# Optimization experiments

Measured on AMD Instinct MI355X. Metric: run time of the kernel, lower is better.

Reference implementation:

```python
import jax, jax.numpy as jnp
import numpy as np

D_MODEL = 256
NUM_ENTRIES = 256 * 256 * 2  # (a, b, carry_in) table
INPUT_DIM = 2 * D_MODEL + 2


def _build_tables():
    k = np.arange(NUM_ENTRIES)
    a = k // 512
    b = (k // 2) % 256
    c = k % 2
    W1 = np.zeros((INPUT_DIM, NUM_ENTRIES), dtype=np.float32)
    W1[a, k] = 1.0
    W1[D_MODEL + b, k] = 1.0
    W1[2 * D_MODEL + c, k] = 1.0
    total = a + b + c
    W2_sum = np.zeros((NUM_ENTRIES, D_MODEL), dtype=np.float32)
    W2_sum[k, total & 255] = 1.0
    W2_carry = np.zeros((NUM_ENTRIES, 2), dtype=np.float32)
    W2_carry[k, (total >= 256).astype(np.int64)] = 1.0
    return jnp.asarray(W1), jnp.asarray(W2_sum), jnp.asarray(W2_carry)


def setup_inputs() -> dict:
    key = jax.random.key(0)
    k1, k2 = jax.random.split(key)
    W1, W2_sum, W2_carry = _build_tables()
    a_emb = jax.random.uniform(k1, (4, D_MODEL), dtype=jnp.float32)
    b_emb = jax.random.uniform(k2, (4, D_MODEL), dtype=jnp.float32)
    return {"a_emb": a_emb, "b_emb": b_emb, "W1": W1, "W2_sum": W2_sum, "W2_carry": W2_carry}


def reference(a_emb, b_emb, W1, W2_sum, W2_carry):
    # 4 sequential carry-propagation steps over the bytes of a 32-bit add.
    def step(carry, ab):
        a_i, b_i = ab  # each [D_MODEL]
        x = jnp.concatenate([a_i, b_i, carry])  # [514]
        scores = x @ W1  # [131072] matvec against full table
        weights = jax.nn.softmax((scores - 2.5) * 10.0)  # sharp soft one-hot
        result = weights @ W2_sum   # [D_MODEL]
        new_carry = weights @ W2_carry  # [2]
        return new_carry, result

    carry0 = jnp.zeros(2, dtype=a_emb.dtype).at[0].set(1.0)
    _, results = jax.lax.scan(step, carry0, (a_emb, b_emb))
    return results  # [4, D_MODEL]
```

## Files before the change

### kernel.cpp

```cpp
#include <hip/hip_runtime.h>

__global__ __launch_bounds__(256) void c4_adder_kernel(
    const float* __restrict__ a_emb,
    const float* __restrict__ b_emb,
    float* __restrict__ out)
{
    __shared__ __align__(16) float sEA[256];
    __shared__ __align__(16) float sEB2[512];
    __shared__ __align__(16) float sPartT[4][256];
    __shared__ float sConv[256];
    __shared__ float sRed[8];

    const int tid = threadIdx.x;
    const int l   = tid & 63;
    const int w   = tid >> 6;

    float carry0 = 1.0f, carry1 = 0.0f;

    for (int step = 0; step < 4; ++step) {
        const float ea = expf(10.0f * a_emb[step * 256 + tid]);
        const float eb = expf(10.0f * b_emb[step * 256 + tid]);
        sEA[tid]        = ea;
        sEB2[tid]       = eb;
        sEB2[tid + 256] = eb;
        __syncthreads();

        const float4* EA4 = reinterpret_cast<const float4*>(sEA);
        const float4* EB4 = reinterpret_cast<const float4*>(sEB2);

        float accT0=0.f, accT1=0.f, accT2=0.f, accT3=0.f;
        float accW0=0.f, accW1=0.f, accW2=0.f, accW3=0.f;

        const int m0 = w * 16;
        float4 q1 = EB4[l - m0 + 64];
        #pragma unroll
        for (int mm = 0; mm < 16; ++mm) {
            const int m = m0 + mm;
            const float4 A  = EA4[m];
            const float4 q0 = EB4[l - m + 63];
            const float mGT = (m >  l) ? 1.0f : 0.0f;
            const float mGE = (m >= l) ? 1.0f : 0.0f;
            float p;
            p = A.x*q1.x; accT0 += p; accW0 = fmaf(p, mGT, accW0);
            p = A.y*q0.w; accT0 += p; accW0 = fmaf(p, mGE, accW0);
            p = A.z*q0.z; accT0 += p; accW0 = fmaf(p, mGE, accW0);
            p = A.w*q0.y; accT0 += p; accW0 = fmaf(p, mGE, accW0);
            p = A.x*q1.y; accT1 += p; accW1 = fmaf(p, mGT, accW1);
            p = A.y*q1.x; accT1 += p; accW1 = fmaf(p, mGT, accW1);
            p = A.z*q0.w; accT1 += p; accW1 = fmaf(p, mGE, accW1);
            p = A.w*q0.z; accT1 += p; accW1 = fmaf(p, mGE, accW1);
            p = A.x*q1.z; accT2 += p; accW2 = fmaf(p, mGT, accW2);
            p = A.y*q1.y; accT2 += p; accW2 = fmaf(p, mGT, accW2);
            p = A.z*q1.x; accT2 += p; accW2 = fmaf(p, mGT, accW2);
            p = A.w*q0.w; accT2 += p; accW2 = fmaf(p, mGE, accW2);
            p = A.x*q1.w; accT3 += p; accW3 = fmaf(p, mGT, accW3);
            p = A.y*q1.z; accT3 += p; accW3 = fmaf(p, mGT, accW3);
            p = A.z*q1.y; accT3 += p; accW3 = fmaf(p, mGT, accW3);
            p = A.w*q1.x; accT3 += p; accW3 = fmaf(p, mGT, accW3);
            q1 = q0;
        }

        reinterpret_cast<float4*>(&sPartT[w][0])[l] =
            make_float4(accT0, accT1, accT2, accT3);

        float rc = accT0 + accT1 + accT2 + accT3;
        float rw = accW0 + accW1 + accW2 + accW3;
        #pragma unroll
        for (int off = 32; off > 0; off >>= 1) {
            rc += __shfl_xor(rc, off, 64);
            rw += __shfl_xor(rw, off, 64);
        }
        if (l == 0) { sRed[w] = rc; sRed[4 + w] = rw; }
        __syncthreads();

        const float convT = sPartT[0][tid] + sPartT[1][tid]
                          + sPartT[2][tid] + sPartT[3][tid];
        sConv[tid] = convT;
        const float SC = sRed[0] + sRed[1] + sRed[2] + sRed[3];
        const float SW = sRed[4] + sRed[5] + sRed[6] + sRed[7];
        __syncthreads();

        const float convPrev = sConv[(tid + 255) & 255];
        const float conv255  = sConv[255];

        const float EC0 = expf(10.0f * carry0);
        const float EC1 = expf(10.0f * carry1);
        const float Z   = SC * (EC0 + EC1);

        out[step * 256 + tid] = (EC0 * convT + EC1 * convPrev) / Z;

        const float C1num = EC0 * SW + EC1 * (SW + conv255);
        carry1 = C1num / Z;
        carry0 = (Z - C1num) / Z;
    }
}

extern "C" void kernel_launch(void* const* d_in, const int* in_sizes, int n_in,
                              void* d_out, int out_size, void* d_ws, size_t ws_size,
                              hipStream_t stream) {
    const float* a_emb = (const float*)d_in[0];
    const float* b_emb = (const float*)d_in[1];
    float* out = (float*)d_out;
    (void)in_sizes; (void)n_in; (void)out_size; (void)d_ws; (void)ws_size;
    c4_adder_kernel<<<dim3(1), dim3(256), 0, stream>>>(a_emb, b_emb, out);
}
```

Before: 16.41 us.

## Compute all four steps' convolutions in parallel with 1024 threads, serial carry only at end

The kernel now launches 1024 threads, with each group of 256 handling one byte step. All four convolutions and reductions run concurrently, and the cheap carry recurrence is replayed serially per thread at the end, so the sequential dependency no longer blocks the heavy work. The masked carry-weight sum is also replaced by a suffix-sum formulation (suffix sums of EB times EA), which roughly halves the inner-loop arithmetic. This costs more shared memory, a larger block and redundant carry recomputation in every thread.

```diff
diff --git a/kernel.cpp b/kernel.cpp
--- a/kernel.cpp
+++ b/kernel.cpp
@@ -1,98 +1,100 @@
 #include <hip/hip_runtime.h>
 
-__global__ __launch_bounds__(256) void c4_adder_kernel(
+__global__ __launch_bounds__(1024) void c4_adder_kernel(
     const float* __restrict__ a_emb,
     const float* __restrict__ b_emb,
     float* __restrict__ out)
 {
-    __shared__ __align__(16) float sEA[256];
-    __shared__ __align__(16) float sEB2[512];
-    __shared__ __align__(16) float sPartT[4][256];
-    __shared__ float sConv[256];
-    __shared__ float sRed[8];
+    __shared__ __align__(16) float sEA[4][256];
+    __shared__ __align__(16) float sEB2[4][512];
+    __shared__ __align__(16) float sPart[4][4][256];
+    __shared__ __align__(16) float sConv[4][256];
+    __shared__ float sWT[4][4];
+    __shared__ float sRedC[4][4];
+    __shared__ float sRedW[4][4];
 
     const int tid = threadIdx.x;
+    const int s   = tid >> 8;
+    const int j   = tid & 255;
+    const int w4  = j >> 6;
     const int l   = tid & 63;
-    const int w   = tid >> 6;
 
-    float carry0 = 1.0f, carry1 = 0.0f;
+    const float ea = expf(10.0f * a_emb[tid]);
+    const float eb = expf(10.0f * b_emb[tid]);
+    sEA[s][j]        = ea;
+    sEB2[s][j]       = eb;
+    sEB2[s][j + 256] = eb;
 
-    for (int step = 0; step < 4; ++step) {
-        const float ea = expf(10.0f * a_emb[step * 256 + tid]);
-        const float eb = expf(10.0f * b_emb[step * 256 + tid]);
-        sEA[tid]        = ea;
-        sEB2[tid]       = eb;
-        sEB2[tid + 256] = eb;
-        __syncthreads();
+    float suf = eb;
+    #pragma unroll
+    for (int off = 1; off < 64; off <<= 1) {
+        const float u = __shfl_down(suf, off, 64);
+        if (l + off < 64) suf += u;
+    }
+    if (l == 0) sWT[s][w4] = suf;
+    __syncthreads();
 
-        const float4* EA4 = reinterpret_cast<const float4*>(sEA);
-        const float4* EB4 = reinterpret_cast<const float4*>(sEB2);
+    for (int w = w4 + 1; w < 4; ++w) suf += sWT[s][w];
+    const float term = (j > 0) ? sEA[s][256 - j] * suf : 0.0f;
 
-        float accT0=0.f, accT1=0.f, accT2=0.f, accT3=0.f;
-        float accW0=0.f, accW1=0.f, accW2=0.f, accW3=0.f;
+    const float4* EA4 = reinterpret_cast<const float4*>(&sEA[s][0]);
+    const float4* EB4 = reinterpret_cast<const float4*>(&sEB2[s][0]);
+    float t0 = 0.f, t1 = 0.f, t2 = 0.f, t3 = 0.f;
+    const int m0 = w4 * 16;
+    float4 q1 = EB4[l - m0 + 64];
+    #pragma unroll
+    for (int mm = 0; mm < 16; ++mm) {
+        const int m = m0 + mm;
+        const float4 A  = EA4[m];
+        const float4 q0 = EB4[l - m + 63];
+        t0 = fmaf(A.x, q1.x, t0); t0 = fmaf(A.y, q0.w, t0);
+        t0 = fmaf(A.z, q0.z, t0); t0 = fmaf(A.w, q0.y, t0);
+        t1 = fmaf(A.x, q1.y, t1); t1 = fmaf(A.y, q1.x, t1);
+        t1 = fmaf(A.z, q0.w, t1); t1 = fmaf(A.w, q0.z, t1);
+        t2 = fmaf(A.x, q1.z, t2); t2 = fmaf(A.y, q1.y, t2);
+        t2 = fmaf(A.z, q1.x, t2); t2 = fmaf(A.w, q0.w, t2);
+        t3 = fmaf(A.x, q1.w, t3); t3 = fmaf(A.y, q1.z, t3);
+        t3 = fmaf(A.z, q1.y, t3); t3 = fmaf(A.w, q1.x, t3);
+        q1 = q0;
+    }
+    reinterpret_cast<float4*>(&sPart[s][w4][0])[l] = make_float4(t0, t1, t2, t3);
 
-        const int m0 = w * 16;
-        float4 q1 = EB4[l - m0 + 64];
-        #pragma unroll
-        for (int mm = 0; mm < 16; ++mm) {
-            const int m = m0 + mm;
-            const float4 A  = EA4[m];
-            const float4 q0 = EB4[l - m + 63];
-            const float mGT = (m >  l) ? 1.0f : 0.0f;
-            const float mGE = (m >= l) ? 1.0f : 0.0f;
-            float p;
-            p = A.x*q1.x; accT0 += p; accW0 = fmaf(p, mGT, accW0);
-            p = A.y*q0.w; accT0 += p; accW0 = fmaf(p, mGE, accW0);
-            p = A.z*q0.z; accT0 += p; accW0 = fmaf(p, mGE, accW0);
-            p = A.w*q0.y; accT0 += p; accW0 = fmaf(p, mGE, accW0);
-            p = A.x*q1.y; accT1 += p; accW1 = fmaf(p, mGT, accW1);
-            p = A.y*q1.x; accT1 += p; accW1 = fmaf(p, mGT, accW1);
-            p = A.z*q0.w; accT1 += p; accW1 = fmaf(p, mGE, accW1);
-            p = A.w*q0.z; accT1 += p; accW1 = fmaf(p, mGE, accW1);
-            p = A.x*q1.z; accT2 += p; accW2 = fmaf(p, mGT, accW2);
-            p = A.y*q1.y; accT2 += p; accW2 = fmaf(p, mGT, accW2);
-            p = A.z*q1.x; accT2 += p; accW2 = fmaf(p, mGT, accW2);
-            p = A.w*q0.w; accT2 += p; accW2 = fmaf(p, mGE, accW2);
-            p = A.x*q1.w; accT3 += p; accW3 = fmaf(p, mGT, accW3);
-            p = A.y*q1.z; accT3 += p; accW3 = fmaf(p, mGT, accW3);
-            p = A.z*q1.y; accT3 += p; accW3 = fmaf(p, mGT, accW3);
-            p = A.w*q1.x; accT3 += p; accW3 = fmaf(p, mGT, accW3);
-            q1 = q0;
-        }
+    float rc = t0 + t1 + t2 + t3;
+    float rw = term;
+    #pragma unroll
+    for (int off = 32; off; off >>= 1) {
+        rc += __shfl_xor(rc, off, 64);
+        rw += __shfl_xor(rw, off, 64);
+    }
+    if (l == 0) { sRedC[s][w4] = rc; sRedW[s][w4] = rw; }
+    __syncthreads();
 
-        reinterpret_cast<float4*>(&sPartT[w][0])[l] =
-            make_float4(accT0, accT1, accT2, accT3);
+    const float convT = sPart[s][0][j] + sPart[s][1][j]
+                      + sPart[s][2][j] + sPart[s][3][j];
+    sConv[s][j] = convT;
+    __syncthreads();
 
-        float rc = accT0 + accT1 + accT2 + accT3;
-        float rw = accW0 + accW1 + accW2 + accW3;
-        #pragma unroll
-        for (int off = 32; off > 0; off >>= 1) {
-            rc += __shfl_xor(rc, off, 64);
-            rw += __shfl_xor(rw, off, 64);
-        }
-        if (l == 0) { sRed[w] = rc; sRed[4 + w] = rw; }
-        __syncthreads();
+    float SC_[4], SW_[4], C255_[4];
+    #pragma unroll
+    for (int ss = 0; ss < 4; ++ss) {
+        SC_[ss]   = sRedC[ss][0] + sRedC[ss][1] + sRedC[ss][2] + sRedC[ss][3];
+        SW_[ss]   = sRedW[ss][0] + sRedW[ss][1] + sRedW[ss][2] + sRedW[ss][3];
+        C255_[ss] = sConv[ss][255];
+    }
+    const float convPrev = sConv[s][(j + 255) & 255];
 
-        const float convT = sPartT[0][tid] + sPartT[1][tid]
-                          + sPartT[2][tid] + sPartT[3][tid];
-        sConv[tid] = convT;
-        const float SC = sRed[0] + sRed[1] + sRed[2] + sRed[3];
-        const float SW = sRed[4] + sRed[5] + sRed[6] + sRed[7];
-        __syncthreads();
-
-        const float convPrev = sConv[(tid + 255) & 255];
-        const float conv255  = sConv[255];
-
-        const float EC0 = expf(10.0f * carry0);
-        const float EC1 = expf(10.0f * carry1);
-        const float Z   = SC * (EC0 + EC1);
-
-        out[step * 256 + tid] = (EC0 * convT + EC1 * convPrev) / Z;
-
-        const float C1num = EC0 * SW + EC1 * (SW + conv255);
-        carry1 = C1num / Z;
-        carry0 = (Z - C1num) / Z;
+    float c0 = 1.0f, c1 = 0.0f, myout = 0.0f;
+    #pragma unroll
+    for (int ss = 0; ss < 4; ++ss) {
+        const float EC0 = expf(10.0f * c0);
+        const float EC1 = expf(10.0f * c1);
+        const float Z   = SC_[ss] * (EC0 + EC1);
+        if (ss == s) myout = (EC0 * convT + EC1 * convPrev) / Z;
+        const float C1num = EC0 * SW_[ss] + EC1 * (SW_[ss] + C255_[ss]);
+        c1 = C1num / Z;
+        c0 = (Z - C1num) / Z;
     }
+    out[tid] = myout;
 }
 
 extern "C" void kernel_launch(void* const* d_in, const int* in_sizes, int n_in,
@@ -102,5 +104,5 @@
     const float* b_emb = (const float*)d_in[1];
     float* out = (float*)d_out;
     (void)in_sizes; (void)n_in; (void)out_size; (void)d_ws; (void)ws_size;
-    c4_adder_kernel<<<dim3(1), dim3(256), 0, stream>>>(a_emb, b_emb, out);
+    c4_adder_kernel<<<dim3(1), dim3(1024), 0, stream>>>(a_emb, b_emb, out);
 }
```

After: 13.15 us. -19.8%, faster.
